# Optimization experiments

Hardware: AMD Instinct MI355X
Metric: run time of the kernel (lower is better)

Reference implementation:

```python
import jax, jax.numpy as jnp
import numpy as np

D_MODEL = 1024
N_HEADS = 16
D_HEAD = D_MODEL // N_HEADS
D_FF = 4096
ACT_BITS = 8
GSIZE = 64
EPS = 1e-6


def act_quant(x):
    # per-group int8 activation quantization with straight-through estimator
    qmax = 2.0 ** (ACT_BITS - 1) - 1.0  # 127
    g = x.reshape(x.shape[:-1] + (-1, GSIZE))
    s = jnp.clip(jnp.max(jnp.abs(g), axis=-1, keepdims=True), 1e-5, None) / qmax
    q = jnp.clip(jnp.round(g / s), -qmax, qmax) * s
    out = g + jax.lax.stop_gradient(q - g)  # STE
    return out.reshape(x.shape)


def weight_quant_1b(w):
    # binarize to sign(w) * mean(|w|), STE
    alpha = jnp.mean(jnp.abs(w))
    wq = jnp.sign(w) * alpha
    return w + jax.lax.stop_gradient(wq - w)


def bitlinear(x, w):
    # y = Q_act(x) @ Q_w(w)^T ; w is [out, in]
    return act_quant(x) @ weight_quant_1b(w).T


def rmsnorm(x, g):
    return x * jax.lax.rsqrt(jnp.mean(x * x, axis=-1, keepdims=True) + EPS) * g


def causal_sdpa(q, k, v):
    # q,k,v: [B,H,T,Dh]
    T = q.shape[2]
    scores = jnp.einsum('bhqd,bhkd->bhqk', q, k) / jnp.sqrt(jnp.asarray(D_HEAD, q.dtype))
    mask = jnp.tril(jnp.ones((T, T), dtype=bool))
    scores = jnp.where(mask, scores, jnp.asarray(-1e30, q.dtype))
    p = jax.nn.softmax(scores, axis=-1)
    return jnp.einsum('bhqk,bhkd->bhqd', p, v)


def setup_inputs() -> dict:
    key = jax.random.key(0)
    ks = jax.random.split(key, 11)
    sd = 0.02
    inp = {
        'x': jax.random.normal(ks[0], (1, 4096, D_MODEL), dtype=jnp.float32),
        'wq': jax.random.normal(ks[1], (D_MODEL, D_MODEL), dtype=jnp.float32) * sd,
        'wk': jax.random.normal(ks[2], (D_MODEL, D_MODEL), dtype=jnp.float32) * sd,
        'wv': jax.random.normal(ks[3], (D_MODEL, D_MODEL), dtype=jnp.float32) * sd,
        'wo': jax.random.normal(ks[4], (D_MODEL, D_MODEL), dtype=jnp.float32) * sd,
        'w1': jax.random.normal(ks[5], (D_FF, D_MODEL), dtype=jnp.float32) * sd,
        'w2': jax.random.normal(ks[6], (D_FF, D_MODEL), dtype=jnp.float32) * sd,
        'w3': jax.random.normal(ks[7], (D_MODEL, D_FF), dtype=jnp.float32) * sd,
        'g1': jnp.ones((D_MODEL,), dtype=jnp.float32),
        'g2': jnp.ones((D_MODEL,), dtype=jnp.float32),
    }
    return inp


def reference(x, wq, wk, wv, wo, w1, w2, w3, g1, g2):
    B, T, C = x.shape
    # attention branch
    h = rmsnorm(x, g1)
    q = bitlinear(h, wq).reshape(B, T, N_HEADS, D_HEAD).transpose(0, 2, 1, 3)
    k = bitlinear(h, wk).reshape(B, T, N_HEADS, D_HEAD).transpose(0, 2, 1, 3)
    v = bitlinear(h, wv).reshape(B, T, N_HEADS, D_HEAD).transpose(0, 2, 1, 3)
    y = causal_sdpa(q, k, v).transpose(0, 2, 1, 3).reshape(B, T, C)
    x = x + bitlinear(y, wo)
    # SwiGLU FFN branch
    h2 = rmsnorm(x, g2)
    ff = bitlinear(jax.nn.silu(bitlinear(h2, w1)) * bitlinear(h2, w2), w3)
    return x + ff
```

## Files before the change

### kernel.cpp

```cpp
#include <hip/hip_runtime.h>
#include <math.h>


typedef unsigned short u16;
typedef __attribute__((ext_vector_type(4))) float f32x4;
typedef __attribute__((ext_vector_type(4))) unsigned short u16x4;
typedef __attribute__((ext_vector_type(8))) unsigned short u16x8;
typedef __attribute__((ext_vector_type(8))) __bf16 bf16x8;

#define DEV static __device__ __forceinline__

DEV float bf2f(u16 u) { union { unsigned i; float f; } c; c.i = ((unsigned)u) << 16; return c.f; }
DEV u16 f2bf(float f) { __bf16 b = (__bf16)f; return __builtin_bit_cast(u16, b); }
DEV float fexp2(float x) { float r; asm("v_exp_f32 %0, %1" : "=v"(r) : "v"(x)); return r; }

DEV void gload16(const void* g, void* l) {
  __builtin_amdgcn_global_load_lds((__attribute__((address_space(1))) void*)g,
                                   (__attribute__((address_space(3))) void*)l,
                                   16, 0, 0);
}

__global__ __launch_bounds__(256) void convert_sign_all(
    const float* __restrict__ w0, const float* __restrict__ w1,
    const float* __restrict__ w2, const float* __restrict__ w3,
    const float* __restrict__ w4, const float* __restrict__ w5,
    const float* __restrict__ w6, u16* __restrict__ sgn_base,
    float* __restrict__ partial,
    const float* __restrict__ x, const float* __restrict__ g1,
    u16* __restrict__ hq) {
  __shared__ float red[4];
  const int wi = blockIdx.y;
  const int t = threadIdx.x;

  if (wi == 7) {
#pragma unroll 1
    for (int rr = 0; rr < 16; ++rr) {
      const int row = blockIdx.x * 16 + rr;
      f32x4 v = ((const f32x4*)(x + (size_t)row * 1024))[t];
      float ss = v[0] * v[0] + v[1] * v[1] + v[2] * v[2] + v[3] * v[3];
#pragma unroll
      for (int off = 32; off >= 1; off >>= 1) ss += __shfl_xor(ss, off);
      if ((t & 63) == 0) red[t >> 6] = ss;
      __syncthreads();
      float tot = red[0] + red[1] + red[2] + red[3];
      __syncthreads();
      float rinv = rsqrtf(tot * (1.f / 1024.f) + 1e-6f);
      f32x4 gg = ((const f32x4*)g1)[t];
      float n[4];
#pragma unroll
      for (int j = 0; j < 4; ++j) n[j] = v[j] * rinv * gg[j];
      float gm = fmaxf(fmaxf(fabsf(n[0]), fabsf(n[1])), fmaxf(fabsf(n[2]), fabsf(n[3])));
#pragma unroll
      for (int off = 1; off <= 8; off <<= 1) gm = fmaxf(gm, __shfl_xor(gm, off));
      float s = fmaxf(gm, 1e-5f) / 127.0f;
      u16x4 o;
#pragma unroll
      for (int j = 0; j < 4; ++j) {
        float q = fminf(fmaxf(rintf(n[j] / s), -127.f), 127.f) * s;
        o[j] = f2bf(q);
      }
      ((u16x4*)hq)[(size_t)row * 256 + t] = o;
    }
    return;
  }

  const float* srcs[7] = {w0, w1, w2, w3, w4, w5, w6};
  const size_t offs[7] = {0, 1048576, 2097152, 3145728, 4194304, 4194304, 12582912};
  const float* w = srcs[wi];
  u16* sgn = sgn_base + offs[wi];
  const int n4 = (wi < 4) ? 262144 : 1048576;
  const bool ilv = (wi == 4) || (wi == 5);
  const int ilv_add = (wi == 5) ? 16 : 0;

  float s = 0.f;
  for (int i = blockIdx.x * 256 + t; i < n4; i += 256 * 256) {
    f32x4 v = ((const f32x4*)w)[i];
    u16x4 o;
#pragma unroll
    for (int j = 0; j < 4; ++j) {
      float f = v[j];
      o[j] = f > 0.f ? (u16)0x3F80 : (f < 0.f ? (u16)0xBF80 : (u16)0);
      s += fabsf(f);
    }
    size_t di = i;
    if (ilv) {
      int e = i << 2;
      int row = e >> 10, col = e & 1023;
      int dst = ((row >> 4) << 5) + ilv_add + (row & 15);
      di = ((size_t)dst << 8) + (col >> 2);
    }
    ((u16x4*)sgn)[di] = o;
  }
#pragma unroll
  for (int off = 32; off >= 1; off >>= 1) s += __shfl_xor(s, off);
  if ((t & 63) == 0) red[t >> 6] = s;
  __syncthreads();
  if (t == 0)
    partial[wi * 256 + blockIdx.x] = red[0] + red[1] + red[2] + red[3];
}

__global__ __launch_bounds__(256) void finalize_alpha(
    const float* __restrict__ partial, float* __restrict__ alphas) {
  __shared__ float red[4];
  int wi = blockIdx.x;
  float v = partial[wi * 256 + threadIdx.x];
#pragma unroll
  for (int off = 32; off >= 1; off >>= 1) v += __shfl_xor(v, off);
  if ((threadIdx.x & 63) == 0) red[threadIdx.x >> 6] = v;
  __syncthreads();
  if (threadIdx.x == 0)
    alphas[wi] = (red[0] + red[1] + red[2] + red[3]) *
                 (wi < 4 ? (1.f / 1048576.f) : (1.f / 4194304.f));
}

__global__ __launch_bounds__(256) void rmsnorm_quant(
    const float* __restrict__ x, const float* __restrict__ g, u16* __restrict__ out) {
  __shared__ float red[4];
  const int row = blockIdx.x, t = threadIdx.x;
  f32x4 v = ((const f32x4*)(x + (size_t)row * 1024))[t];
  float ss = v[0] * v[0] + v[1] * v[1] + v[2] * v[2] + v[3] * v[3];
#pragma unroll
  for (int off = 32; off >= 1; off >>= 1) ss += __shfl_xor(ss, off);
  if ((t & 63) == 0) red[t >> 6] = ss;
  __syncthreads();
  float tot = red[0] + red[1] + red[2] + red[3];
  float rinv = rsqrtf(tot * (1.f / 1024.f) + 1e-6f);
  f32x4 gg = ((const f32x4*)g)[t];
  float n[4];
#pragma unroll
  for (int j = 0; j < 4; ++j) n[j] = v[j] * rinv * gg[j];
  float gm = fmaxf(fmaxf(fabsf(n[0]), fabsf(n[1])), fmaxf(fabsf(n[2]), fabsf(n[3])));
#pragma unroll
  for (int off = 1; off <= 8; off <<= 1) gm = fmaxf(gm, __shfl_xor(gm, off));
  float s = fmaxf(gm, 1e-5f) / 127.0f;
  u16x4 o;
#pragma unroll
  for (int j = 0; j < 4; ++j) {
    float q = fminf(fmaxf(rintf(n[j] / s), -127.f), 127.f) * s;
    o[j] = f2bf(q);
  }
  ((u16x4*)out)[(size_t)row * 256 + t] = o;
}

__global__ __launch_bounds__(256) void transpose_v(
    const u16* __restrict__ qkv, u16* __restrict__ Vt) {
  __shared__ u16 T[64][65];
  const int tt = blockIdx.x, h = blockIdx.y, tid = threadIdx.x;
#pragma unroll
  for (int i = 0; i < 2; ++i) {
    int idx = i * 2048 + tid * 8;
    int trow = idx >> 6, dcol = idx & 63;
    u16x8 v = *(const u16x8*)(qkv + (size_t)(tt * 64 + trow) * 3072 + 2048 + h * 64 + dcol);
#pragma unroll
    for (int j = 0; j < 8; ++j) T[dcol + j][trow] = v[j];
  }
  __syncthreads();
#pragma unroll
  for (int i = 0; i < 2; ++i) {
    int idx = i * 2048 + tid * 8;
    int drow = idx >> 6, tcol = idx & 63;
    u16x8 v;
#pragma unroll
    for (int j = 0; j < 8; ++j) v[j] = T[drow][tcol + j];
    *(u16x8*)(Vt + ((size_t)h * 64 + drow) * 4096 + tt * 64 + tcol) = v;
  }
}

template <bool RES, int BM>
__global__ __launch_bounds__(256) void gemm_bt(
    const u16* __restrict__ A, const u16* __restrict__ B,
    const float* __restrict__ alpha, int ashift, const float* __restrict__ res,
    void* __restrict__ Cout, int M, int N, int K) {
  constexpr int NI = (BM == 128) ? 4 : 2;
  constexpr int WNE = (BM == 128) ? 64 : 32;
  __shared__ u16 As[BM * 64];
  __shared__ u16 Bs[128 * 64];
  const int tid = threadIdx.x;
  const int l = tid & 63, w = tid >> 6;
  const int wm = (BM == 128) ? (w >> 1) : 0;
  const int wn = (BM == 128) ? (w & 1) : w;
  const int lr = l & 15, lg = l >> 4;
  const int xorv = (l & 7) << 4;
  const int brow = blockIdx.y * BM;
  const int bcol = blockIdx.x * 128;
  const int src_chunk = (l & 7) ^ (l >> 3);
  const int rl = w * 8 + (l >> 3);

  f32x4 acc[4][NI];
#pragma unroll
  for (int i = 0; i < 4; ++i)
#pragma unroll
    for (int j = 0; j < NI; ++j) acc[i][j] = (f32x4){0.f, 0.f, 0.f, 0.f};

  const char* Ag = (const char*)A;
  const char* Bg = (const char*)B;
  const int nkt = K >> 6;
  for (int kt = 0; kt < nkt; ++kt) {
    __syncthreads();
    const size_t kb = (size_t)kt * 128 + src_chunk * 16;
#pragma unroll
    for (int it = 0; it < BM / 32; ++it)
      gload16(Ag + (size_t)(brow + it * 32 + rl) * (size_t)(K * 2) + kb,
              &As[(it * 32 + w * 8) * 64]);
#pragma unroll
    for (int it = 0; it < 4; ++it)
      gload16(Bg + (size_t)(bcol + it * 32 + rl) * (size_t)(K * 2) + kb,
              &Bs[(it * 32 + w * 8) * 64]);
    __syncthreads();

    bf16x8 af[4][2], bfr[NI][2];
#pragma unroll
    for (int mi = 0; mi < 4; ++mi)
#pragma unroll
      for (int ks = 0; ks < 2; ++ks) {
        int row = wm * 64 + mi * 16 + lr;
        af[mi][ks] = *(const bf16x8*)((const char*)As + row * 128 + ((ks * 64 + lg * 16) ^ xorv));
      }
#pragma unroll
    for (int ni = 0; ni < NI; ++ni)
#pragma unroll
      for (int ks = 0; ks < 2; ++ks) {
        int row = wn * WNE + ni * 16 + lr;
        bfr[ni][ks] = *(const bf16x8*)((const char*)Bs + row * 128 + ((ks * 64 + lg * 16) ^ xorv));
      }
#pragma unroll
    for (int ks = 0; ks < 2; ++ks)
#pragma unroll
      for (int mi = 0; mi < 4; ++mi)
#pragma unroll
        for (int ni = 0; ni < NI; ++ni)
          acc[mi][ni] = __builtin_amdgcn_mfma_f32_16x16x32_bf16(
              af[mi][ks], bfr[ni][ks], acc[mi][ni], 0, 0, 0);
  }

  const float scale = alpha[bcol >> ashift];
#pragma unroll
  for (int mi = 0; mi < 4; ++mi)
#pragma unroll
    for (int ni = 0; ni < NI; ++ni)
#pragma unroll
      for (int r = 0; r < 4; ++r) {
        int row = brow + wm * 64 + mi * 16 + lg * 4 + r;
        int col = bcol + wn * WNE + ni * 16 + lr;
        float vv = acc[mi][ni][r] * scale;
        if (RES)
          ((float*)Cout)[(size_t)row * N + col] = res[(size_t)row * N + col] + vv;
        else
          ((u16*)Cout)[(size_t)row * N + col] = f2bf(vv);
      }
}

__global__ __launch_bounds__(256, 2) void gemm_ffn(
    const u16* __restrict__ A, const u16* __restrict__ B12,
    const float* __restrict__ alpha2, u16* __restrict__ zq) {
  __shared__ u16 As[256 * 64];
  __shared__ u16 Bs[128 * 64];
  const int tid = threadIdx.x;
  const int l = tid & 63, w = tid >> 6;
  const int wm = w >> 1, wn = w & 1;
  const int lr = l & 15, lg = l >> 4;
  const int xorv = (l & 7) << 4;
  const int brow = blockIdx.y * 256;
  const int bcol = blockIdx.x * 128;
  const int src_chunk = (l & 7) ^ (l >> 3);
  const int rl = w * 8 + (l >> 3);

  f32x4 acc[8][4];
#pragma unroll
  for (int i = 0; i < 8; ++i)
#pragma unroll
    for (int j = 0; j < 4; ++j) acc[i][j] = (f32x4){0.f, 0.f, 0.f, 0.f};

  for (int kt = 0; kt < 16; ++kt) {
    __syncthreads();
    const size_t kb = (size_t)kt * 128 + src_chunk * 16;
#pragma unroll
    for (int it = 0; it < 8; ++it)
      gload16((const char*)A + (size_t)(brow + it * 32 + rl) * 2048 + kb,
              &As[(it * 32 + w * 8) * 64]);
#pragma unroll
    for (int it = 0; it < 4; ++it)
      gload16((const char*)B12 + (size_t)(bcol + it * 32 + rl) * 2048 + kb,
              &Bs[(it * 32 + w * 8) * 64]);
    __syncthreads();

#pragma unroll
    for (int ks = 0; ks < 2; ++ks) {
      bf16x8 bfr[4];
#pragma unroll
      for (int ni = 0; ni < 4; ++ni)
        bfr[ni] = *(const bf16x8*)((const char*)Bs + (wn * 64 + ni * 16 + lr) * 128 +
                                   ((ks * 64 + lg * 16) ^ xorv));
#pragma unroll
      for (int mi = 0; mi < 8; ++mi) {
        bf16x8 af = *(const bf16x8*)((const char*)As + (wm * 128 + mi * 16 + lr) * 128 +
                                     ((ks * 64 + lg * 16) ^ xorv));
#pragma unroll
        for (int ni = 0; ni < 4; ++ni)
          acc[mi][ni] = __builtin_amdgcn_mfma_f32_16x16x32_bf16(
              af, bfr[ni], acc[mi][ni], 0, 0, 0);
      }
    }
  }

  const float a1 = alpha2[0], a2 = alpha2[1];
  const float L2E = 1.4426950408889634f;
  float zl[8][4], zh[8][4], rm[8][4];
#pragma unroll
  for (int mi = 0; mi < 8; ++mi)
#pragma unroll
    for (int r = 0; r < 4; ++r) {
      float y1 = acc[mi][0][r] * a1;
      zl[mi][r] = y1 / (1.f + fexp2(-L2E * y1)) * (acc[mi][1][r] * a2);
      float y3 = acc[mi][2][r] * a1;
      zh[mi][r] = y3 / (1.f + fexp2(-L2E * y3)) * (acc[mi][3][r] * a2);
      float g = fmaxf(fabsf(zl[mi][r]), fabsf(zh[mi][r]));
#pragma unroll
      for (int off = 1; off <= 8; off <<= 1) g = fmaxf(g, __shfl_xor(g, off));
      rm[mi][r] = g;
    }

  float* rmax = (float*)&As[0];
  __syncthreads();
  if (lr == 0) {
#pragma unroll
    for (int mi = 0; mi < 8; ++mi)
#pragma unroll
      for (int r = 0; r < 4; ++r)
        rmax[w * 128 + mi * 16 + lg * 4 + r] = rm[mi][r];
  }
  __syncthreads();

#pragma unroll
  for (int mi = 0; mi < 8; ++mi)
#pragma unroll
    for (int r = 0; r < 4; ++r) {
      float g = fmaxf(rm[mi][r], rmax[(w ^ 1) * 128 + mi * 16 + lg * 4 + r]);
      float gmc = fmaxf(g, 1e-5f);
      float s = gmc * (1.f / 127.f);
      float inv = 127.f / gmc;
      int row = brow + wm * 128 + mi * 16 + lg * 4 + r;
      int zc = blockIdx.x * 64 + wn * 32 + lr;
      float q0 = fminf(fmaxf(rintf(zl[mi][r] * inv), -127.f), 127.f) * s;
      float q1 = fminf(fmaxf(rintf(zh[mi][r] * inv), -127.f), 127.f) * s;
      zq[(size_t)row * 4096 + zc] = f2bf(q0);
      zq[(size_t)row * 4096 + zc + 16] = f2bf(q1);
    }
}

__global__ __launch_bounds__(256) void attn_kernel(
    const u16* __restrict__ QKV, const u16* __restrict__ Vt, u16* __restrict__ Y) {
  __shared__ u16 Ks[2][64 * 64];
  __shared__ u16 Vs[2][64 * 64];
  __shared__ u16 Ps[4][16 * 64];

  const int tid = threadIdx.x;
  const int l = tid & 63, w = tid >> 6;
  const int lr = l & 15, lg = l >> 4;
  const int xorv = (l & 7) << 4;
  const int h = blockIdx.x;
  const int y = blockIdx.y;
  const int qt = (y < 32) ? y : (95 - y);
  const int src_chunk = (l & 7) ^ (l >> 3);
  const int rl = w * 8 + (l >> 3);
  const float SC = 0.18033688f;

  const int qrow0 = qt * 64 + w * 16;
  const int nkt = qt + 1;

  bf16x8 qf[2];
#pragma unroll
  for (int ks = 0; ks < 2; ++ks)
    qf[ks] = __builtin_bit_cast(
        bf16x8, *(const u16x8*)(QKV + (size_t)(qrow0 + lr) * 3072 +
                                h * 64 + ks * 32 + lg * 8));

  f32x4 O[4];
#pragma unroll
  for (int ni = 0; ni < 4; ++ni) O[ni] = (f32x4){0.f, 0.f, 0.f, 0.f};
  float m_ = -3e38f, lsum = 0.f;

  auto STAGE = [&](int buf, int kt) {
#pragma unroll
    for (int it = 0; it < 2; ++it) {
      int krow = kt * 64 + it * 32 + rl;
      gload16((const char*)QKV + ((size_t)krow * 3072 + 1024 + h * 64) * 2 + src_chunk * 16,
              &Ks[buf][(it * 32 + w * 8) * 64]);
      int drow = it * 32 + rl;
      gload16((const char*)Vt + (((size_t)h * 64 + drow) * 4096 + kt * 64) * 2 + src_chunk * 16,
              &Vs[buf][(it * 32 + w * 8) * 64]);
    }
  };

  STAGE(0, 0);
#pragma unroll 1
  for (int kt = 0; kt < nkt; ++kt) {
    const int cur = kt & 1;
    if (kt + 1 < nkt) {
      STAGE(cur ^ 1, kt + 1);
      asm volatile("s_waitcnt vmcnt(4)" ::: "memory");
    } else {
      asm volatile("s_waitcnt vmcnt(0)" ::: "memory");
    }
    __builtin_amdgcn_s_barrier();
    __builtin_amdgcn_sched_barrier(0);

    const char* kbase = (const char*)&Ks[cur][0];
    const char* vbase = (const char*)&Vs[cur][0];

    f32x4 S[4];
    __builtin_amdgcn_s_setprio(1);
#pragma unroll
    for (int ni = 0; ni < 4; ++ni) {
      S[ni] = (f32x4){0.f, 0.f, 0.f, 0.f};
#pragma unroll
      for (int ks = 0; ks < 2; ++ks) {
        bf16x8 kf = *(const bf16x8*)(kbase + (ni * 16 + lr) * 128 +
                                     ((ks * 64 + lg * 16) ^ xorv));
        S[ni] = __builtin_amdgcn_mfma_f32_16x16x32_bf16(kf, qf[ks], S[ni], 0, 0, 0);
      }
    }
    __builtin_amdgcn_s_setprio(0);

#pragma unroll
    for (int ni = 0; ni < 4; ++ni)
#pragma unroll
      for (int r = 0; r < 4; ++r) S[ni][r] *= SC;
    if (kt == qt) {
#pragma unroll
      for (int ni = 0; ni < 4; ++ni)
#pragma unroll
        for (int r = 0; r < 4; ++r)
          if ((ni * 16 + lg * 4 + r) > (w * 16 + lr)) S[ni][r] = -3e38f;
    }

    float nm = -3e38f;
#pragma unroll
    for (int ni = 0; ni < 4; ++ni)
#pragma unroll
      for (int r = 0; r < 4; ++r) nm = fmaxf(nm, S[ni][r]);
    nm = fmaxf(nm, __shfl_xor(nm, 16));
    nm = fmaxf(nm, __shfl_xor(nm, 32));
    if (__ballot(nm > m_ + 8.f)) {
      float mn = fmaxf(m_, nm);
      float fac = fexp2(m_ - mn);
      m_ = mn;
      lsum *= fac;
#pragma unroll
      for (int ni = 0; ni < 4; ++ni) O[ni] *= fac;
    }
    float rs = 0.f;
#pragma unroll
    for (int ni = 0; ni < 4; ++ni)
#pragma unroll
      for (int r = 0; r < 4; ++r) {
        float pv = fexp2(S[ni][r] - m_);
        S[ni][r] = pv;
        rs += pv;
      }
    rs += __shfl_xor(rs, 16);
    rs += __shfl_xor(rs, 32);
    lsum += rs;

#pragma unroll
    for (int ni = 0; ni < 4; ++ni) {
      u16x4 pk;
#pragma unroll
      for (int r = 0; r < 4; ++r) pk[r] = f2bf(S[ni][r]);
      *(u16x4*)((char*)&Ps[w][0] + lr * 128 + ((ni * 32 + lg * 8) ^ xorv)) = pk;
    }
    bf16x8 pt[2];
#pragma unroll
    for (int ks = 0; ks < 2; ++ks)
      pt[ks] = *(const bf16x8*)((const char*)&Ps[w][0] + lr * 128 +
                                ((ks * 64 + lg * 16) ^ xorv));

    __builtin_amdgcn_s_setprio(1);
#pragma unroll
    for (int ni = 0; ni < 4; ++ni) {
#pragma unroll
      for (int ks = 0; ks < 2; ++ks) {
        bf16x8 vf = *(const bf16x8*)(vbase + (ni * 16 + lr) * 128 +
                                     ((ks * 64 + lg * 16) ^ xorv));
        O[ni] = __builtin_amdgcn_mfma_f32_16x16x32_bf16(vf, pt[ks], O[ni], 0, 0, 0);
      }
    }
    __builtin_amdgcn_s_setprio(0);
    asm volatile("" ::: "memory");
    __builtin_amdgcn_s_barrier();
  }

  float rinv = 1.f / lsum;
  float o[4][4];
  float gm = 0.f;
#pragma unroll
  for (int ni = 0; ni < 4; ++ni)
#pragma unroll
    for (int r = 0; r < 4; ++r) {
      o[ni][r] = O[ni][r] * rinv;
      gm = fmaxf(gm, fabsf(o[ni][r]));
    }
  gm = fmaxf(gm, __shfl_xor(gm, 16));
  gm = fmaxf(gm, __shfl_xor(gm, 32));
  float gmc = fmaxf(gm, 1e-5f);
  float s = gmc * (1.f / 127.f);
  float inv = 127.f / gmc;
#pragma unroll
  for (int ni = 0; ni < 4; ++ni) {
    u16x4 ov;
#pragma unroll
    for (int r = 0; r < 4; ++r) {
      float q = fminf(fmaxf(rintf(o[ni][r] * inv), -127.f), 127.f) * s;
      ov[r] = f2bf(q);
    }
    *(u16x4*)(Y + (size_t)(qrow0 + lr) * 1024 + h * 64 + ni * 16 + lg * 4) = ov;
  }
}

extern "C" void kernel_launch(void* const* d_in, const int* in_sizes, int n_in,
                              void* d_out, int out_size, void* d_ws, size_t ws_size,
                              hipStream_t stream) {
  const float* x  = (const float*)d_in[0];
  const float* wq = (const float*)d_in[1];
  const float* wk = (const float*)d_in[2];
  const float* wv = (const float*)d_in[3];
  const float* wo = (const float*)d_in[4];
  const float* w1 = (const float*)d_in[5];
  const float* w2 = (const float*)d_in[6];
  const float* w3 = (const float*)d_in[7];
  const float* g1 = (const float*)d_in[8];
  const float* g2 = (const float*)d_in[9];

  char* ws = (char*)d_ws;
  const size_t MB = 1024 * 1024;
  u16* sgn   = (u16*)ws;
  u16* sWq   = (u16*)(ws + 0 * MB);
  u16* sWo   = (u16*)(ws + 6 * MB);
  u16* sW12  = (u16*)(ws + 8 * MB);
  u16* sW3   = (u16*)(ws + 24 * MB);
  float* partial = (float*)(ws + 32 * MB);
  float* alphas  = (float*)(ws + 32 * MB + 16384);
  u16* Vt    = (u16*)(ws + 33 * MB);
  float* x1  = (float*)(ws + 33 * MB);
  u16* hq    = (u16*)(ws + 49 * MB);
  u16* qkv   = (u16*)(ws + 57 * MB);
  u16* yb    = (u16*)(ws + 81 * MB);
  u16* zq    = (u16*)(ws + 57 * MB);

  convert_sign_all<<<dim3(256, 8), 256, 0, stream>>>(wq, wk, wv, wo, w1, w2, w3,
                                                     sgn, partial, x, g1, hq);
  finalize_alpha<<<7, 256, 0, stream>>>(partial, alphas);

  gemm_bt<false, 128><<<dim3(24, 32), 256, 0, stream>>>(hq, sWq, alphas, 10, nullptr,
                                                        qkv, 4096, 3072, 1024);
  transpose_v<<<dim3(64, 16), 256, 0, stream>>>(qkv, Vt);
  attn_kernel<<<dim3(16, 64), 256, 0, stream>>>(qkv, Vt, yb);
  gemm_bt<true, 64><<<dim3(8, 64), 256, 0, stream>>>(yb, sWo, alphas + 3, 31, x,
                                                     x1, 4096, 1024, 1024);
  rmsnorm_quant<<<4096, 256, 0, stream>>>(x1, g2, hq);
  gemm_ffn<<<dim3(64, 16), 256, 0, stream>>>(hq, sW12, alphas + 4, zq);
  gemm_bt<true, 64><<<dim3(8, 64), 256, 0, stream>>>(zq, sW3, alphas + 6, 31, x1,
                                                     (float*)d_out, 4096, 1024, 4096);
}
```

Before: 309.6 us.

## Use larger GEMM tiles for QKV projection and 128-row attention blocks

Adds a gemm_fat kernel with 256x128 tiles for the QKV projection, which halves the grid and raises reuse per loaded tile. Attention now uses 512-thread blocks covering 128 query rows, so each K/V tile staged into shared memory serves eight waves instead of four. The softmax scale is folded into an fma before the exp, and a packed bf16 convert replaces scalar conversions. The cost is fewer blocks, which means less occupancy and coarser causal load balancing, and gemm_fat has no double buffering.

Measured after the change: 307.4 us. About the same (-0.7%).

```diff
diff --git a/kernel.cpp b/kernel.cpp
--- a/kernel.cpp
+++ b/kernel.cpp
@@ -3,6 +3,8 @@
 
 
 typedef unsigned short u16;
+typedef unsigned int u32;
+typedef __attribute__((ext_vector_type(2))) unsigned int u32x2;
 typedef __attribute__((ext_vector_type(4))) float f32x4;
 typedef __attribute__((ext_vector_type(4))) unsigned short u16x4;
 typedef __attribute__((ext_vector_type(8))) unsigned short u16x8;
@@ -13,6 +15,9 @@
 DEV float bf2f(u16 u) { union { unsigned i; float f; } c; c.i = ((unsigned)u) << 16; return c.f; }
 DEV u16 f2bf(float f) { __bf16 b = (__bf16)f; return __builtin_bit_cast(u16, b); }
 DEV float fexp2(float x) { float r; asm("v_exp_f32 %0, %1" : "=v"(r) : "v"(x)); return r; }
+DEV u32 cvtpk(float lo, float hi) {
+  u32 r; asm("v_cvt_pk_bf16_f32 %0, %1, %2" : "=v"(r) : "v"(lo), "v"(hi)); return r;
+}
 
 DEV void gload16(const void* g, void* l) {
   __builtin_amdgcn_global_load_lds((__attribute__((address_space(1))) void*)g,
@@ -250,6 +255,79 @@
       }
 }
 
+template <bool RES>
+__global__ __launch_bounds__(256, 2) void gemm_fat(
+    const u16* __restrict__ A, const u16* __restrict__ B,
+    const float* __restrict__ alpha, int ashift, const float* __restrict__ res,
+    void* __restrict__ Cout, int M, int N, int K) {
+  __shared__ u16 As[256 * 64];
+  __shared__ u16 Bs[128 * 64];
+  const int tid = threadIdx.x;
+  const int l = tid & 63, w = tid >> 6;
+  const int wm = w >> 1, wn = w & 1;
+  const int lr = l & 15, lg = l >> 4;
+  const int xorv = (l & 7) << 4;
+  const int brow = blockIdx.y * 256;
+  const int bcol = blockIdx.x * 128;
+  const int src_chunk = (l & 7) ^ (l >> 3);
+  const int rl = w * 8 + (l >> 3);
+
+  f32x4 acc[8][4];
+#pragma unroll
+  for (int i = 0; i < 8; ++i)
+#pragma unroll
+    for (int j = 0; j < 4; ++j) acc[i][j] = (f32x4){0.f, 0.f, 0.f, 0.f};
+
+  const int nkt = K >> 6;
+  for (int kt = 0; kt < nkt; ++kt) {
+    __syncthreads();
+    const size_t kb = (size_t)kt * 128 + src_chunk * 16;
+#pragma unroll
+    for (int it = 0; it < 8; ++it)
+      gload16((const char*)A + (size_t)(brow + it * 32 + rl) * (size_t)(K * 2) + kb,
+              &As[(it * 32 + w * 8) * 64]);
+#pragma unroll
+    for (int it = 0; it < 4; ++it)
+      gload16((const char*)B + (size_t)(bcol + it * 32 + rl) * (size_t)(K * 2) + kb,
+              &Bs[(it * 32 + w * 8) * 64]);
+    __syncthreads();
+
+#pragma unroll
+    for (int ks = 0; ks < 2; ++ks) {
+      bf16x8 bfr[4];
+#pragma unroll
+      for (int ni = 0; ni < 4; ++ni)
+        bfr[ni] = *(const bf16x8*)((const char*)Bs + (wn * 64 + ni * 16 + lr) * 128 +
+                                   ((ks * 64 + lg * 16) ^ xorv));
+#pragma unroll
+      for (int mi = 0; mi < 8; ++mi) {
+        bf16x8 af = *(const bf16x8*)((const char*)As + (wm * 128 + mi * 16 + lr) * 128 +
+                                     ((ks * 64 + lg * 16) ^ xorv));
+#pragma unroll
+        for (int ni = 0; ni < 4; ++ni)
+          acc[mi][ni] = __builtin_amdgcn_mfma_f32_16x16x32_bf16(
+              af, bfr[ni], acc[mi][ni], 0, 0, 0);
+      }
+    }
+  }
+
+  const float scale = alpha[bcol >> ashift];
+#pragma unroll
+  for (int mi = 0; mi < 8; ++mi)
+#pragma unroll
+    for (int ni = 0; ni < 4; ++ni)
+#pragma unroll
+      for (int r = 0; r < 4; ++r) {
+        int row = brow + wm * 128 + mi * 16 + lg * 4 + r;
+        int col = bcol + wn * 64 + ni * 16 + lr;
+        float vv = acc[mi][ni][r] * scale;
+        if (RES)
+          ((float*)Cout)[(size_t)row * N + col] = res[(size_t)row * N + col] + vv;
+        else
+          ((u16*)Cout)[(size_t)row * N + col] = f2bf(vv);
+      }
+}
+
 __global__ __launch_bounds__(256, 2) void gemm_ffn(
     const u16* __restrict__ A, const u16* __restrict__ B12,
     const float* __restrict__ alpha2, u16* __restrict__ zq) {
@@ -348,11 +426,11 @@
     }
 }
 
-__global__ __launch_bounds__(256) void attn_kernel(
+__global__ __launch_bounds__(512) void attn_kernel(
     const u16* __restrict__ QKV, const u16* __restrict__ Vt, u16* __restrict__ Y) {
   __shared__ u16 Ks[2][64 * 64];
   __shared__ u16 Vs[2][64 * 64];
-  __shared__ u16 Ps[4][16 * 64];
+  __shared__ u16 Ps[8][16 * 64];
 
   const int tid = threadIdx.x;
   const int l = tid & 63, w = tid >> 6;
@@ -360,13 +438,13 @@
   const int xorv = (l & 7) << 4;
   const int h = blockIdx.x;
   const int y = blockIdx.y;
-  const int qt = (y < 32) ? y : (95 - y);
+  const int qt = (y < 16) ? y : (47 - y);
   const int src_chunk = (l & 7) ^ (l >> 3);
   const int rl = w * 8 + (l >> 3);
   const float SC = 0.18033688f;
 
-  const int qrow0 = qt * 64 + w * 16;
-  const int nkt = qt + 1;
+  const int qrow0 = qt * 128 + w * 16;
+  const int nkt = 2 * qt + 2;
 
   bf16x8 qf[2];
 #pragma unroll
@@ -381,15 +459,11 @@
   float m_ = -3e38f, lsum = 0.f;
 
   auto STAGE = [&](int buf, int kt) {
-#pragma unroll
-    for (int it = 0; it < 2; ++it) {
-      int krow = kt * 64 + it * 32 + rl;
-      gload16((const char*)QKV + ((size_t)krow * 3072 + 1024 + h * 64) * 2 + src_chunk * 16,
-              &Ks[buf][(it * 32 + w * 8) * 64]);
-      int drow = it * 32 + rl;
-      gload16((const char*)Vt + (((size_t)h * 64 + drow) * 4096 + kt * 64) * 2 + src_chunk * 16,
-              &Vs[buf][(it * 32 + w * 8) * 64]);
-    }
+    int krow = kt * 64 + rl;
+    gload16((const char*)QKV + ((size_t)krow * 3072 + 1024 + h * 64) * 2 + src_chunk * 16,
+            &Ks[buf][(w * 8) * 64]);
+    gload16((const char*)Vt + (((size_t)h * 64 + rl) * 4096 + kt * 64) * 2 + src_chunk * 16,
+            &Vs[buf][(w * 8) * 64]);
   };
 
   STAGE(0, 0);
@@ -398,7 +472,7 @@
     const int cur = kt & 1;
     if (kt + 1 < nkt) {
       STAGE(cur ^ 1, kt + 1);
-      asm volatile("s_waitcnt vmcnt(4)" ::: "memory");
+      asm volatile("s_waitcnt vmcnt(2)" ::: "memory");
     } else {
       asm volatile("s_waitcnt vmcnt(0)" ::: "memory");
     }
@@ -422,16 +496,13 @@
     }
     __builtin_amdgcn_s_setprio(0);
 
-#pragma unroll
-    for (int ni = 0; ni < 4; ++ni)
-#pragma unroll
-      for (int r = 0; r < 4; ++r) S[ni][r] *= SC;
-    if (kt == qt) {
+    const int tb = kt * 64;
+    if (tb + 63 > qrow0) {
 #pragma unroll
       for (int ni = 0; ni < 4; ++ni)
 #pragma unroll
         for (int r = 0; r < 4; ++r)
-          if ((ni * 16 + lg * 4 + r) > (w * 16 + lr)) S[ni][r] = -3e38f;
+          if (tb + ni * 16 + lg * 4 + r > qrow0 + lr) S[ni][r] = -3e38f;
     }
 
     float nm = -3e38f;
@@ -441,8 +512,9 @@
       for (int r = 0; r < 4; ++r) nm = fmaxf(nm, S[ni][r]);
     nm = fmaxf(nm, __shfl_xor(nm, 16));
     nm = fmaxf(nm, __shfl_xor(nm, 32));
-    if (__ballot(nm > m_ + 8.f)) {
-      float mn = fmaxf(m_, nm);
+    float nms = nm * SC;
+    if (__ballot(nms > m_ + 8.f)) {
+      float mn = fmaxf(m_, nms);
       float fac = fexp2(m_ - mn);
       m_ = mn;
       lsum *= fac;
@@ -454,7 +526,7 @@
     for (int ni = 0; ni < 4; ++ni)
 #pragma unroll
       for (int r = 0; r < 4; ++r) {
-        float pv = fexp2(S[ni][r] - m_);
+        float pv = fexp2(__builtin_fmaf(S[ni][r], SC, -m_));
         S[ni][r] = pv;
         rs += pv;
       }
@@ -464,10 +536,10 @@
 
 #pragma unroll
     for (int ni = 0; ni < 4; ++ni) {
-      u16x4 pk;
-#pragma unroll
-      for (int r = 0; r < 4; ++r) pk[r] = f2bf(S[ni][r]);
-      *(u16x4*)((char*)&Ps[w][0] + lr * 128 + ((ni * 32 + lg * 8) ^ xorv)) = pk;
+      u32x2 pk;
+      pk[0] = cvtpk(S[ni][0], S[ni][1]);
+      pk[1] = cvtpk(S[ni][2], S[ni][3]);
+      *(u32x2*)((char*)&Ps[w][0] + lr * 128 + ((ni * 32 + lg * 8) ^ xorv)) = pk;
     }
     bf16x8 pt[2];
 #pragma unroll
@@ -551,10 +623,10 @@
                                                      sgn, partial, x, g1, hq);
   finalize_alpha<<<7, 256, 0, stream>>>(partial, alphas);
 
-  gemm_bt<false, 128><<<dim3(24, 32), 256, 0, stream>>>(hq, sWq, alphas, 10, nullptr,
-                                                        qkv, 4096, 3072, 1024);
+  gemm_fat<false><<<dim3(24, 16), 256, 0, stream>>>(hq, sWq, alphas, 10, nullptr,
+                                                    qkv, 4096, 3072, 1024);
   transpose_v<<<dim3(64, 16), 256, 0, stream>>>(qkv, Vt);
-  attn_kernel<<<dim3(16, 64), 256, 0, stream>>>(qkv, Vt, yb);
+  attn_kernel<<<dim3(16, 32), 512, 0, stream>>>(qkv, Vt, yb);
   gemm_bt<true, 64><<<dim3(8, 64), 256, 0, stream>>>(yb, sWo, alphas + 3, 31, x,
                                                      x1, 4096, 1024, 1024);
   rmsnorm_quant<<<4096, 256, 0, stream>>>(x1, g2, hq);
```
